# Optimization experiments

Measured on AMD Instinct MI355X. Metric: run time of the kernel, lower is better.

The kernel has to match this reference:

```python
import jax, jax.numpy as jnp
import numpy as np

B, N, D = 4, 4096, 1024

def setup_inputs() -> dict:
    key = jax.random.key(0)
    kx, kql, kqr, kk, kv = jax.random.split(key, 5)
    std = 1.0 / D
    return {
        "x": jax.random.normal(kx, (B, N, D), dtype=jnp.float32),
        "w_query_left": jax.random.normal(kql, (D, D), dtype=jnp.float32) * std,
        "w_query_right": jax.random.normal(kqr, (D, D), dtype=jnp.float32) * std,
        "w_key": jax.random.normal(kk, (D, D), dtype=jnp.float32) * std,
        "w_value": jax.random.normal(kv, (D, D), dtype=jnp.float32) * std,
    }

def reference(x, w_query_left, w_query_right, w_key, w_value):
    # Four dxd projections
    query_left = jnp.einsum('bnd,de->bne', x, w_query_left)
    query_right = jnp.einsum('bnd,de->bne', x, w_query_right)
    key = jnp.einsum('bnd,de->bne', x, w_key)
    value = jnp.einsum('bnd,de->bne', x, w_value)
    # Elementwise gate
    query = query_left * query_right
    # Kernelized attention: key^T @ value, then query @ kv  (dropout p=0 in eval)
    kv_attn = jnp.einsum('bnd,bne->bde', key, value)   # [B, D, D]
    linear_attn = jnp.einsum('bnd,bde->bne', query, kv_attn)
    return linear_attn
```

## Files before the change

### kernel.cpp

```cpp
#include <hip/hip_runtime.h>
#include <stdint.h>

typedef short bf16x8 __attribute__((ext_vector_type(8)));
typedef float f32x4 __attribute__((ext_vector_type(4)));

__device__ __forceinline__ uint16_t f2b(float f) {
    uint32_t u = __builtin_bit_cast(uint32_t, f);
    return (uint16_t)((u + 0x7fffu + ((u >> 16) & 1u)) >> 16);
}

__device__ __forceinline__ void gll16(const void* g, void* l) {
    __builtin_amdgcn_global_load_lds(
        (const __attribute__((address_space(1))) uint32_t*)(uintptr_t)g,
        (__attribute__((address_space(3))) uint32_t*)(uint32_t)(uintptr_t)l,
        16, 0, 0);
}

__device__ __forceinline__ void swz3(int& bx, int& by, int& bz) {
    const int nx = gridDim.x, ny = gridDim.y, nz = gridDim.z;
    const int n = nx * ny * nz;
    int orig = blockIdx.x + nx * (blockIdx.y + ny * blockIdx.z);
    int l = (orig & 7) * (n >> 3) + (orig >> 3);
    bx = l % nx; l /= nx;
    by = l % ny;
    bz = l / ny;
}

struct Ptr4 { const float* p[4]; };

__global__ __launch_bounds__(256) void prep(const float* __restrict__ x,
                                            uint16_t* __restrict__ xb,
                                            uint16_t* __restrict__ xT,
                                            Ptr4 wp, uint16_t* __restrict__ Wt) {
    __shared__ uint16_t tile[64][68];
    const int t = threadIdx.x;
    int id = blockIdx.x;
    if (id < 4096) {
        const int d0 = (id & 15) * 64;
        const int n0 = ((id >> 4) & 63) * 64;
        const int b = id >> 10;
        const float* xbase = x + (size_t)b * 4194304;
#pragma unroll
        for (int p = 0; p < 4; p++) {
            int row = p * 16 + (t >> 4);
            int c4 = (t & 15) * 4;
            float4 v = *(const float4*)&xbase[(size_t)(n0 + row) * 1024 + d0 + c4];
            uint16_t b0 = f2b(v.x), b1 = f2b(v.y), b2 = f2b(v.z), b3 = f2b(v.w);
            tile[row][c4 + 0] = b0;
            tile[row][c4 + 1] = b1;
            tile[row][c4 + 2] = b2;
            tile[row][c4 + 3] = b3;
            uint2 pk;
            pk.x = (uint32_t)b0 | ((uint32_t)b1 << 16);
            pk.y = (uint32_t)b2 | ((uint32_t)b3 << 16);
            *(uint2*)&xb[(size_t)(b * 4096 + n0 + row) * 1024 + d0 + c4] = pk;
        }
        __syncthreads();
        uint16_t* oT = xT + (size_t)b * 4194304;
#pragma unroll
        for (int p = 0; p < 4; p++) {
            int a = p * 16 + (t >> 4);
            int b4 = (t & 15) * 4;
            uint32_t x0 = tile[b4 + 0][a], x1 = tile[b4 + 1][a];
            uint32_t x2 = tile[b4 + 2][a], x3 = tile[b4 + 3][a];
            uint2 pk;
            pk.x = x0 | (x1 << 16);
            pk.y = x2 | (x3 << 16);
            *(uint2*)&oT[(size_t)(d0 + a) * 4096 + n0 + b4] = pk;
        }
    } else {
        id -= 4096;
        const int c0 = (id & 15) * 64;
        const int r0 = ((id >> 4) & 15) * 64;
        const int m = id >> 8;
        const float* in = wp.p[m];
        uint16_t* o = Wt + (size_t)m * 1048576;
#pragma unroll
        for (int p = 0; p < 4; p++) {
            int row = p * 16 + (t >> 4);
            int c4 = (t & 15) * 4;
            float4 v = *(const float4*)&in[(size_t)(r0 + row) * 1024 + c0 + c4];
            tile[row][c4 + 0] = f2b(v.x);
            tile[row][c4 + 1] = f2b(v.y);
            tile[row][c4 + 2] = f2b(v.z);
            tile[row][c4 + 3] = f2b(v.w);
        }
        __syncthreads();
#pragma unroll
        for (int p = 0; p < 4; p++) {
            int a = p * 16 + (t >> 4);
            int b4 = (t & 15) * 4;
            uint32_t x0 = tile[b4 + 0][a], x1 = tile[b4 + 1][a];
            uint32_t x2 = tile[b4 + 2][a], x3 = tile[b4 + 3][a];
            uint2 pk;
            pk.x = x0 | (x1 << 16);
            pk.y = x2 | (x3 << 16);
            *(uint2*)&o[(size_t)(c0 + a) * 1024 + r0 + b4] = pk;
        }
    }
}

__global__ __launch_bounds__(512, 2) void proj_gate8(const uint16_t* __restrict__ A,
                                                     const uint16_t* __restrict__ Wt,
                                                     uint16_t* __restrict__ Q) {
    __shared__ uint16_t lds[65536];
    const int t = threadIdx.x;
    const int wave = t >> 6;
    const int lane = t & 63;
    int bx, by, bz;
    swz3(bx, by, bz);
    const int m0 = by * 256;
    const int e0 = bx * 128;
    const uint16_t* B1 = Wt + (size_t)e0 * 1024;
    const uint16_t* B2 = Wt + 1048576 + (size_t)e0 * 1024;
    const int wm = (wave >> 1) * 64;
    const int wn = (wave & 1) * 64;

    int LsA0 = t * 16;
    int LsA1 = 8192 + t * 16;
    int gbA0 = LsA0 ^ (((LsA0 >> 7) & 7) << 4);
    int gbA1 = LsA1 ^ (((LsA1 >> 7) & 7) << 4);
    int gbB  = gbA0;
    const uint16_t* srcA0 = A + (size_t)(m0 + (gbA0 >> 6)) * 1024 + ((gbA0 & 63) >> 1);
    const uint16_t* srcA1 = A + (size_t)(m0 + (gbA1 >> 6)) * 1024 + ((gbA1 & 63) >> 1);
    const uint16_t* srcB1 = B1 + (size_t)(gbB >> 6) * 1024 + ((gbB & 63) >> 1);
    const uint16_t* srcB2 = B2 + (size_t)(gbB >> 6) * 1024 + ((gbB & 63) >> 1);

    auto STAGE = [&](int kt_, int ks_) {
        const int h = (2 * kt_ + ks_) & 3;
        const int kb = kt_ * 64 + ks_ * 32;
        uint16_t* db = lds + h * 16384 + (wave << 9);
        gll16(srcA0 + kb, db);
        gll16(srcA1 + kb, db + 4096);
        gll16(srcB1 + kb, db + 8192);
        gll16(srcB2 + kb, db + 12288);
    };

    const int cb = (lane >> 4) << 4;
    int aoff[4], b1off[4], b2off[4];
#pragma unroll
    for (int i = 0; i < 4; i++) {
        int g = (wm + i * 16 + (lane & 15)) * 64 + cb;
        aoff[i] = (g ^ (((g >> 7) & 7) << 4)) >> 1;
    }
#pragma unroll
    for (int j = 0; j < 4; j++) {
        int g = (wn + j * 16 + (lane & 15)) * 64 + cb;
        int sw = (g ^ (((g >> 7) & 7) << 4)) >> 1;
        b1off[j] = 8192 + sw;
        b2off[j] = 12288 + sw;
    }

    f32x4 acc1[4][4] = {};
    f32x4 acc2[4][4] = {};

    STAGE(0, 0); STAGE(0, 1); STAGE(1, 0); STAGE(1, 1);
    asm volatile("s_waitcnt vmcnt(12)" ::: "memory");
    __builtin_amdgcn_s_barrier();

    for (int kt = 0; kt < 16; ++kt) {
        const uint16_t* lb0 = lds + ((2 * kt) & 3) * 16384;
        const uint16_t* lb1 = lds + ((2 * kt + 1) & 3) * 16384;
        bf16x8 af[4], bq[4];

#pragma unroll
        for (int i = 0; i < 4; i++) af[i] = *(const bf16x8*)&lb0[aoff[i]];
#pragma unroll
        for (int j = 0; j < 4; j++) bq[j] = *(const bf16x8*)&lb0[b1off[j]];
        __builtin_amdgcn_s_barrier();
        asm volatile("s_waitcnt lgkmcnt(0)" ::: "memory");
        __builtin_amdgcn_sched_barrier(0);
        __builtin_amdgcn_s_setprio(1);
#pragma unroll
        for (int i = 0; i < 4; i++)
#pragma unroll
            for (int j = 0; j < 4; j++)
                acc1[i][j] = __builtin_amdgcn_mfma_f32_16x16x32_bf16(af[i], bq[j],
                                                                     acc1[i][j], 0, 0, 0);
        __builtin_amdgcn_s_setprio(0);
        __builtin_amdgcn_s_barrier();

#pragma unroll
        for (int j = 0; j < 4; j++) bq[j] = *(const bf16x8*)&lb0[b2off[j]];
        __builtin_amdgcn_s_barrier();
        asm volatile("s_waitcnt lgkmcnt(0)" ::: "memory");
        __builtin_amdgcn_sched_barrier(0);
        __builtin_amdgcn_s_setprio(1);
#pragma unroll
        for (int i = 0; i < 4; i++)
#pragma unroll
            for (int j = 0; j < 4; j++)
                acc2[i][j] = __builtin_amdgcn_mfma_f32_16x16x32_bf16(af[i], bq[j],
                                                                     acc2[i][j], 0, 0, 0);
        __builtin_amdgcn_s_setprio(0);
        if (kt < 15) { asm volatile("s_waitcnt vmcnt(8)" ::: "memory"); }
        else         { asm volatile("s_waitcnt vmcnt(0)" ::: "memory"); }
        __builtin_amdgcn_s_barrier();
        if (kt < 14) STAGE(kt + 2, 0);

#pragma unroll
        for (int i = 0; i < 4; i++) af[i] = *(const bf16x8*)&lb1[aoff[i]];
#pragma unroll
        for (int j = 0; j < 4; j++) bq[j] = *(const bf16x8*)&lb1[b1off[j]];
        __builtin_amdgcn_s_barrier();
        asm volatile("s_waitcnt lgkmcnt(0)" ::: "memory");
        __builtin_amdgcn_sched_barrier(0);
        __builtin_amdgcn_s_setprio(1);
#pragma unroll
        for (int i = 0; i < 4; i++)
#pragma unroll
            for (int j = 0; j < 4; j++)
                acc1[i][j] = __builtin_amdgcn_mfma_f32_16x16x32_bf16(af[i], bq[j],
                                                                     acc1[i][j], 0, 0, 0);
        __builtin_amdgcn_s_setprio(0);
        __builtin_amdgcn_s_barrier();

#pragma unroll
        for (int j = 0; j < 4; j++) bq[j] = *(const bf16x8*)&lb1[b2off[j]];
        __builtin_amdgcn_s_barrier();
        asm volatile("s_waitcnt lgkmcnt(0)" ::: "memory");
        __builtin_amdgcn_sched_barrier(0);
        __builtin_amdgcn_s_setprio(1);
#pragma unroll
        for (int i = 0; i < 4; i++)
#pragma unroll
            for (int j = 0; j < 4; j++)
                acc2[i][j] = __builtin_amdgcn_mfma_f32_16x16x32_bf16(af[i], bq[j],
                                                                     acc2[i][j], 0, 0, 0);
        __builtin_amdgcn_s_setprio(0);
        if (kt < 14)       { asm volatile("s_waitcnt vmcnt(8)" ::: "memory"); }
        else if (kt == 14) { asm volatile("s_waitcnt vmcnt(4)" ::: "memory"); }
        else               { asm volatile("s_waitcnt vmcnt(0)" ::: "memory"); }
        __builtin_amdgcn_s_barrier();
        if (kt < 14) STAGE(kt + 2, 1);
    }

    const int rl = (lane >> 4) * 4;
    const int cl = lane & 15;
#pragma unroll
    for (int i = 0; i < 4; i++)
#pragma unroll
        for (int j = 0; j < 4; j++)
#pragma unroll
            for (int r = 0; r < 4; r++) {
                float g = acc1[i][j][r] * acc2[i][j][r];
                Q[(size_t)(m0 + wm + i * 16 + rl + r) * 1024 + e0 + wn + j * 16 + cl] = f2b(g);
            }
}

__global__ __launch_bounds__(512, 2) void gram8(const uint16_t* __restrict__ xT,
                                                float* __restrict__ P) {
    __shared__ uint16_t lds[49152];
    const int t = threadIdx.x;
    const int wave = t >> 6;
    const int lane = t & 63;
    int bx, by, bz;
    swz3(bx, by, bz);
    const int m0 = by * 256;
    const int n0 = bx * 128;
    const int batch = bz >> 1, ks = bz & 1;
    const uint16_t* Xb = xT + (size_t)batch * 4194304 + ks * 2048;
    const int wm = (wave >> 1) * 64;
    const int wn = (wave & 1) * 64;

    int LsA0 = t * 16;
    int LsA1 = 8192 + t * 16;
    int gbA0 = LsA0 ^ (((LsA0 >> 7) & 7) << 4);
    int gbA1 = LsA1 ^ (((LsA1 >> 7) & 7) << 4);
    int gbB  = gbA0;
    const uint16_t* srcA0 = Xb + (size_t)(m0 + (gbA0 >> 6)) * 4096 + ((gbA0 & 63) >> 1);
    const uint16_t* srcA1 = Xb + (size_t)(m0 + (gbA1 >> 6)) * 4096 + ((gbA1 & 63) >> 1);
    const uint16_t* srcB  = Xb + (size_t)(n0 + (gbB  >> 6)) * 4096 + ((gbB  & 63) >> 1);

    auto STAGE = [&](int kt_, int ks2_) {
        const int h = (2 * kt_ + ks2_) & 3;
        const int kb = kt_ * 64 + ks2_ * 32;
        uint16_t* db = lds + h * 12288 + (wave << 9);
        gll16(srcA0 + kb, db);
        gll16(srcA1 + kb, db + 4096);
        gll16(srcB  + kb, db + 8192);
    };

    const int cb = (lane >> 4) << 4;
    int aoff[4], boff[4];
#pragma unroll
    for (int i = 0; i < 4; i++) {
        int g = (wm + i * 16 + (lane & 15)) * 64 + cb;
        aoff[i] = (g ^ (((g >> 7) & 7) << 4)) >> 1;
    }
#pragma unroll
    for (int j = 0; j < 4; j++) {
        int g = (wn + j * 16 + (lane & 15)) * 64 + cb;
        boff[j] = 8192 + ((g ^ (((g >> 7) & 7) << 4)) >> 1);
    }

    f32x4 acc[4][4] = {};

    STAGE(0, 0); STAGE(0, 1); STAGE(1, 0); STAGE(1, 1);
    asm volatile("s_waitcnt vmcnt(9)" ::: "memory");
    __builtin_amdgcn_s_barrier();

    for (int kt = 0; kt < 32; ++kt) {
        const uint16_t* lb0 = lds + ((2 * kt) & 3) * 12288;
        const uint16_t* lb1 = lds + ((2 * kt + 1) & 3) * 12288;
        bf16x8 af[4], bq[4];

#pragma unroll
        for (int i = 0; i < 4; i++) af[i] = *(const bf16x8*)&lb0[aoff[i]];
#pragma unroll
        for (int j = 0; j < 4; j++) bq[j] = *(const bf16x8*)&lb0[boff[j]];
        __builtin_amdgcn_s_barrier();
        asm volatile("s_waitcnt lgkmcnt(0)" ::: "memory");
        __builtin_amdgcn_sched_barrier(0);
        __builtin_amdgcn_s_setprio(1);
#pragma unroll
        for (int i = 0; i < 4; i++)
#pragma unroll
            for (int j = 0; j < 4; j++)
                acc[i][j] = __builtin_amdgcn_mfma_f32_16x16x32_bf16(af[i], bq[j],
                                                                    acc[i][j], 0, 0, 0);
        __builtin_amdgcn_s_setprio(0);
        if (kt < 31) { asm volatile("s_waitcnt vmcnt(6)" ::: "memory"); }
        else         { asm volatile("s_waitcnt vmcnt(0)" ::: "memory"); }
        __builtin_amdgcn_s_barrier();
        if (kt < 30) STAGE(kt + 2, 0);

#pragma unroll
        for (int i = 0; i < 4; i++) af[i] = *(const bf16x8*)&lb1[aoff[i]];
#pragma unroll
        for (int j = 0; j < 4; j++) bq[j] = *(const bf16x8*)&lb1[boff[j]];
        __builtin_amdgcn_s_barrier();
        asm volatile("s_waitcnt lgkmcnt(0)" ::: "memory");
        __builtin_amdgcn_sched_barrier(0);
        __builtin_amdgcn_s_setprio(1);
#pragma unroll
        for (int i = 0; i < 4; i++)
#pragma unroll
            for (int j = 0; j < 4; j++)
                acc[i][j] = __builtin_amdgcn_mfma_f32_16x16x32_bf16(af[i], bq[j],
                                                                    acc[i][j], 0, 0, 0);
        __builtin_amdgcn_s_setprio(0);
        if (kt < 30)       { asm volatile("s_waitcnt vmcnt(6)" ::: "memory"); }
        else if (kt == 30) { asm volatile("s_waitcnt vmcnt(3)" ::: "memory"); }
        else               { asm volatile("s_waitcnt vmcnt(0)" ::: "memory"); }
        __builtin_amdgcn_s_barrier();
        if (kt < 30) STAGE(kt + 2, 1);
    }

    float* Pb = P + (size_t)bz * 1048576;
    const int crow = m0 + wm + (lane >> 4) * 4;
    const int ccol = n0 + wn + (lane & 15);
#pragma unroll
    for (int i = 0; i < 4; i++)
#pragma unroll
        for (int j = 0; j < 4; j++)
#pragma unroll
            for (int r = 0; r < 4; r++)
                Pb[(size_t)(crow + i * 16 + r) * 1024 + ccol + j * 16] = acc[i][j][r];
}

__global__ __launch_bounds__(256) void gemm_h(const uint16_t* __restrict__ WvT,
                                              const float* __restrict__ P,
                                              uint16_t* __restrict__ H) {
    int bxs, bys, bzs;
    swz3(bxs, bys, bzs);
    __shared__ uint16_t lA[4096];
    __shared__ uint16_t lB[4096];

    const int t = threadIdx.x;
    const int wave = t >> 6;
    const int lane = t & 63;
    const int m0 = bys * 128;
    const int n0 = bxs * 128;
    const int wm = (wave >> 1) * 64;
    const int wn = (wave & 1) * 64;

    const uint16_t* gA0 = WvT + (size_t)(m0 + (t >> 2)) * 1024 + (t & 3) * 8;
    uint16_t* lA0 = lA + wave * 512;
    uint16_t* lA1 = lA + 2048 + wave * 512;

    const int row1 = n0 + (t >> 2);
    const int row2 = row1 + 64;
    const float* pb1 = P + (size_t)(row1 >> 10) * 2097152 + (size_t)(row1 & 1023) * 1024 + (t & 3) * 8;
    const float* pb2 = P + (size_t)(row2 >> 10) * 2097152 + (size_t)(row2 & 1023) * 1024 + (t & 3) * 8;
    uint16_t* wB1 = lB + (t >> 2) * 32 + (t & 3) * 8;
    uint16_t* wB2 = lB + 2048 + (t >> 2) * 32 + (t & 3) * 8;

    f32x4 acc[4][4] = {};

    const int arow = wm + (lane & 15);
    const int brow = wn + (lane & 15);
    const int koff = (lane >> 4) * 8;

    for (int k0 = 0; k0 < 1024; k0 += 32) {
        __syncthreads();
        gll16(gA0 + k0, lA0);
        gll16(gA0 + (size_t)64 * 1024 + k0, lA1);
        {
            float4 a0 = *(const float4*)(pb1 + k0);
            float4 a1 = *(const float4*)(pb1 + k0 + 4);
            float4 b0 = *(const float4*)(pb1 + 1048576 + k0);
            float4 b1 = *(const float4*)(pb1 + 1048576 + k0 + 4);
            uint4 v;
            v.x = (uint32_t)f2b(a0.x + b0.x) | ((uint32_t)f2b(a0.y + b0.y) << 16);
            v.y = (uint32_t)f2b(a0.z + b0.z) | ((uint32_t)f2b(a0.w + b0.w) << 16);
            v.z = (uint32_t)f2b(a1.x + b1.x) | ((uint32_t)f2b(a1.y + b1.y) << 16);
            v.w = (uint32_t)f2b(a1.z + b1.z) | ((uint32_t)f2b(a1.w + b1.w) << 16);
            *(uint4*)wB1 = v;
        }
        {
            float4 a0 = *(const float4*)(pb2 + k0);
            float4 a1 = *(const float4*)(pb2 + k0 + 4);
            float4 b0 = *(const float4*)(pb2 + 1048576 + k0);
            float4 b1 = *(const float4*)(pb2 + 1048576 + k0 + 4);
            uint4 v;
            v.x = (uint32_t)f2b(a0.x + b0.x) | ((uint32_t)f2b(a0.y + b0.y) << 16);
            v.y = (uint32_t)f2b(a0.z + b0.z) | ((uint32_t)f2b(a0.w + b0.w) << 16);
            v.z = (uint32_t)f2b(a1.x + b1.x) | ((uint32_t)f2b(a1.y + b1.y) << 16);
            v.w = (uint32_t)f2b(a1.z + b1.z) | ((uint32_t)f2b(a1.w + b1.w) << 16);
            *(uint4*)wB2 = v;
        }
        __syncthreads();

        bf16x8 af[4], bfr[4];
#pragma unroll
        for (int i = 0; i < 4; i++)
            af[i] = *(const bf16x8*)&lA[(arow + i * 16) * 32 + koff];
#pragma unroll
        for (int i = 0; i < 4; i++)
            bfr[i] = *(const bf16x8*)&lB[(brow + i * 16) * 32 + koff];
#pragma unroll
        for (int i = 0; i < 4; i++)
#pragma unroll
            for (int j = 0; j < 4; j++)
                acc[i][j] = __builtin_amdgcn_mfma_f32_16x16x32_bf16(af[i], bfr[j],
                                                                    acc[i][j], 0, 0, 0);
    }

    const int crow = m0 + wm + (lane >> 4) * 4;
    const int ccol = n0 + wn + (lane & 15);
#pragma unroll
    for (int i = 0; i < 4; i++)
#pragma unroll
        for (int j = 0; j < 4; j++)
#pragma unroll
            for (int r = 0; r < 4; r++)
                H[(size_t)(crow + i * 16 + r) * 4096 + ccol + j * 16] = f2b(acc[i][j][r]);
}

__global__ __launch_bounds__(512, 2) void gemm_out8(const uint16_t* __restrict__ A,
                                                    const uint16_t* __restrict__ kvT,
                                                    float* __restrict__ C) {
    __shared__ uint16_t lds[65536];
    const int t = threadIdx.x;
    const int wave = t >> 6;
    const int lane = t & 63;
    int bx, by, bz;
    swz3(bx, by, bz);
    const int m0 = by * 256;
    const int n0 = bx * 256;
    const int batch = by >> 4;
    const uint16_t* Bb = kvT + (size_t)batch * 1048576 + (size_t)n0 * 1024;
    const int wm = (wave >> 2) * 128;
    const int wn = (wave & 3) * 64;

    int Ls0 = t * 16;
    int Ls1 = 8192 + t * 16;
    int gb0 = Ls0 ^ (((Ls0 >> 7) & 7) << 4);
    int gb1 = Ls1 ^ (((Ls1 >> 7) & 7) << 4);
    const uint16_t* srcA0 = A + (size_t)(m0 + (gb0 >> 6)) * 1024 + ((gb0 & 63) >> 1);
    const uint16_t* srcA1 = A + (size_t)(m0 + (gb1 >> 6)) * 1024 + ((gb1 & 63) >> 1);
    const uint16_t* srcB0 = Bb + (size_t)(gb0 >> 6) * 1024 + ((gb0 & 63) >> 1);
    const uint16_t* srcB1 = Bb + (size_t)(gb1 >> 6) * 1024 + ((gb1 & 63) >> 1);

    auto STAGE = [&](int kt_, int ks_) {
        const int h = (2 * kt_ + ks_) & 3;
        const int kb = kt_ * 64 + ks_ * 32;
        uint16_t* db = lds + h * 16384 + (wave << 9);
        gll16(srcA0 + kb, db);
        gll16(srcA1 + kb, db + 4096);
        gll16(srcB0 + kb, db + 8192);
        gll16(srcB1 + kb, db + 12288);
    };

    const int cb = (lane >> 4) << 4;
    int aoff[8], boff[4];
#pragma unroll
    for (int i = 0; i < 8; i++) {
        int g = (wm + i * 16 + (lane & 15)) * 64 + cb;
        aoff[i] = (g ^ (((g >> 7) & 7) << 4)) >> 1;
    }
#pragma unroll
    for (int j = 0; j < 4; j++) {
        int g = (wn + j * 16 + (lane & 15)) * 64 + cb;
        boff[j] = 8192 + ((g ^ (((g >> 7) & 7) << 4)) >> 1);
    }

    f32x4 acc[8][4] = {};

    STAGE(0, 0); STAGE(0, 1); STAGE(1, 0); STAGE(1, 1);
    asm volatile("s_waitcnt vmcnt(12)" ::: "memory");
    __builtin_amdgcn_s_barrier();

    for (int kt = 0; kt < 16; ++kt) {
        const uint16_t* lb0 = lds + ((2 * kt) & 3) * 16384;
        const uint16_t* lb1 = lds + ((2 * kt + 1) & 3) * 16384;
        bf16x8 af[8], bq[4];

#pragma unroll
        for (int i = 0; i < 8; i++) af[i] = *(const bf16x8*)&lb0[aoff[i]];
#pragma unroll
        for (int j = 0; j < 4; j++) bq[j] = *(const bf16x8*)&lb0[boff[j]];
        __builtin_amdgcn_s_barrier();
        asm volatile("s_waitcnt lgkmcnt(0)" ::: "memory");
        __builtin_amdgcn_sched_barrier(0);
        __builtin_amdgcn_s_setprio(1);
#pragma unroll
        for (int i = 0; i < 8; i++)
#pragma unroll
            for (int j = 0; j < 4; j++)
                acc[i][j] = __builtin_amdgcn_mfma_f32_16x16x32_bf16(af[i], bq[j],
                                                                    acc[i][j], 0, 0, 0);
        __builtin_amdgcn_s_setprio(0);
        if (kt < 15) { asm volatile("s_waitcnt vmcnt(8)" ::: "memory"); }
        else         { asm volatile("s_waitcnt vmcnt(0)" ::: "memory"); }
        __builtin_amdgcn_s_barrier();
        if (kt < 14) STAGE(kt + 2, 0);

#pragma unroll
        for (int i = 0; i < 8; i++) af[i] = *(const bf16x8*)&lb1[aoff[i]];
#pragma unroll
        for (int j = 0; j < 4; j++) bq[j] = *(const bf16x8*)&lb1[boff[j]];
        __builtin_amdgcn_s_barrier();
        asm volatile("s_waitcnt lgkmcnt(0)" ::: "memory");
        __builtin_amdgcn_sched_barrier(0);
        __builtin_amdgcn_s_setprio(1);
#pragma unroll
        for (int i = 0; i < 8; i++)
#pragma unroll
            for (int j = 0; j < 4; j++)
                acc[i][j] = __builtin_amdgcn_mfma_f32_16x16x32_bf16(af[i], bq[j],
                                                                    acc[i][j], 0, 0, 0);
        __builtin_amdgcn_s_setprio(0);
        if (kt < 14)       { asm volatile("s_waitcnt vmcnt(8)" ::: "memory"); }
        else if (kt == 14) { asm volatile("s_waitcnt vmcnt(4)" ::: "memory"); }
        else               { asm volatile("s_waitcnt vmcnt(0)" ::: "memory"); }
        __builtin_amdgcn_s_barrier();
        if (kt < 14) STAGE(kt + 2, 1);
    }

    const int rl = (lane >> 4) * 4;
    const int cl = lane & 15;
#pragma unroll
    for (int i = 0; i < 8; i++)
#pragma unroll
        for (int j = 0; j < 4; j++)
#pragma unroll
            for (int r = 0; r < 4; r++)
                C[(size_t)(m0 + wm + i * 16 + rl + r) * 1024 + n0 + wn + j * 16 + cl] =
                    acc[i][j][r];
}

__global__ __launch_bounds__(256) void gemm_nt_bf16(const uint16_t* __restrict__ A,
                                                    int lda, int az,
                                                    const uint16_t* __restrict__ Bt,
                                                    int ldb,
                                                    uint16_t* __restrict__ C,
                                                    int ldc, int cz) {
    int bxs, bys, bzs;
    swz3(bxs, bys, bzs);
    const uint16_t* Ab = A + (size_t)bzs * az;
    uint16_t* Cb = C + (size_t)bzs * cz;

    __shared__ uint16_t lA[4096];
    __shared__ uint16_t lB[4096];

    const int t = threadIdx.x;
    const int wave = t >> 6;
    const int lane = t & 63;
    const int m0 = bys * 128;
    const int n0 = bxs * 128;
    const int wm = (wave >> 1) * 64;
    const int wn = (wave & 1) * 64;

    const uint16_t* gA0 = Ab + (size_t)(m0 + (t >> 2)) * lda + (t & 3) * 8;
    const uint16_t* gB0 = Bt + (size_t)(n0 + (t >> 2)) * ldb + (t & 3) * 8;
    uint16_t* lA0 = lA + wave * 512;
    uint16_t* lA1 = lA + 2048 + wave * 512;
    uint16_t* lB0 = lB + wave * 512;
    uint16_t* lB1 = lB + 2048 + wave * 512;

    f32x4 acc[4][4] = {};

    const int arow = wm + (lane & 15);
    const int brow = wn + (lane & 15);
    const int koff = (lane >> 4) * 8;

    for (int k0 = 0; k0 < 1024; k0 += 32) {
        __syncthreads();
        gll16(gA0 + k0, lA0);
        gll16(gA0 + (size_t)64 * lda + k0, lA1);
        gll16(gB0 + k0, lB0);
        gll16(gB0 + (size_t)64 * ldb + k0, lB1);
        __syncthreads();

        bf16x8 af[4], bfr[4];
#pragma unroll
        for (int i = 0; i < 4; i++)
            af[i] = *(const bf16x8*)&lA[(arow + i * 16) * 32 + koff];
#pragma unroll
        for (int i = 0; i < 4; i++)
            bfr[i] = *(const bf16x8*)&lB[(brow + i * 16) * 32 + koff];
#pragma unroll
        for (int i = 0; i < 4; i++)
#pragma unroll
            for (int j = 0; j < 4; j++)
                acc[i][j] = __builtin_amdgcn_mfma_f32_16x16x32_bf16(af[i], bfr[j],
                                                                    acc[i][j], 0, 0, 0);
    }

    const int crow = m0 + wm + (lane >> 4) * 4;
    const int ccol = n0 + wn + (lane & 15);
#pragma unroll
    for (int i = 0; i < 4; i++)
#pragma unroll
        for (int j = 0; j < 4; j++)
#pragma unroll
            for (int r = 0; r < 4; r++)
                Cb[(size_t)(crow + i * 16 + r) * ldc + ccol + j * 16] = f2b(acc[i][j][r]);
}

extern "C" void kernel_launch(void* const* d_in, const int* in_sizes, int n_in,
                              void* d_out, int out_size, void* d_ws, size_t ws_size,
                              hipStream_t stream) {
    const float* x = (const float*)d_in[0];

    uint16_t* ws  = (uint16_t*)d_ws;
    uint16_t* xb  = ws;
    uint16_t* xT  = ws + 16777216;
    uint16_t* Wt  = ws + 33554432;
    uint16_t* Q   = ws + 37748736;
    float*    P   = (float*)(ws + 54525952);
    uint16_t* H   = ws + 75497472;
    uint16_t* kvT = ws + 79691776;

    Ptr4 wp;
    wp.p[0] = (const float*)d_in[1];
    wp.p[1] = (const float*)d_in[2];
    wp.p[2] = (const float*)d_in[3];
    wp.p[3] = (const float*)d_in[4];
    prep<<<5120, 256, 0, stream>>>(x, xb, xT, wp, Wt);

    proj_gate8<<<dim3(8, 64), 512, 0, stream>>>(xb, Wt, Q);

    gram8<<<dim3(8, 4, 8), 512, 0, stream>>>(xT, P);

    gemm_h<<<dim3(32, 8, 1), 256, 0, stream>>>(Wt + 3 * 1048576, P, H);

    gemm_nt_bf16<<<dim3(8, 8, 4), 256, 0, stream>>>(H, 4096, 1024,
                                                    Wt + 2 * 1048576, 1024,
                                                    kvT, 1024, 1048576);

    gemm_out8<<<dim3(4, 64), 512, 0, stream>>>(Q, kvT, (float*)d_out);
}
```

Baseline: 352.3 us.

## Split partial-Gram reduction into separate kernel and reuse generic NT GEMM

The Gram partial-sum reduction and bf16 conversion move out of the gemm_h inner loop into a standalone reduce_kv kernel that writes a bf16 Gram matrix G. The H GEMM then uses the generic gemm_nt_bf16 path, loading both operands into LDS with global_load_lds. This removes the repeated fp32 loads and conversions of P that each tile of the old kernel did, at the cost of one extra launch and an extra write and read of G. The query projection is also split into two launches of half the row range each, which looks like a tail or scheduling experiment.

```diff
diff --git a/kernel.cpp b/kernel.cpp
--- a/kernel.cpp
+++ b/kernel.cpp
@@ -102,14 +102,15 @@
 
 __global__ __launch_bounds__(512, 2) void proj_gate8(const uint16_t* __restrict__ A,
                                                      const uint16_t* __restrict__ Wt,
-                                                     uint16_t* __restrict__ Q) {
+                                                     uint16_t* __restrict__ Q,
+                                                     int mbase) {
     __shared__ uint16_t lds[65536];
     const int t = threadIdx.x;
     const int wave = t >> 6;
     const int lane = t & 63;
     int bx, by, bz;
     swz3(bx, by, bz);
-    const int m0 = by * 256;
+    const int m0 = mbase + by * 256;
     const int e0 = bx * 128;
     const uint16_t* B1 = Wt + (size_t)e0 * 1024;
     const uint16_t* B2 = Wt + 1048576 + (size_t)e0 * 1024;
@@ -359,11 +360,35 @@
                 Pb[(size_t)(crow + i * 16 + r) * 1024 + ccol + j * 16] = acc[i][j][r];
 }
 
-__global__ __launch_bounds__(256) void gemm_h(const uint16_t* __restrict__ WvT,
-                                              const float* __restrict__ P,
-                                              uint16_t* __restrict__ H) {
+__global__ __launch_bounds__(256) void reduce_kv(const float4* __restrict__ P,
+                                                 uint2* __restrict__ G) {
+    int i = blockIdx.x * 256 + threadIdx.x;
+    int b = i >> 18;
+    int r = i & 262143;
+    const float4* base = P + (size_t)b * 524288 + r;
+    float4 s0 = base[0];
+    float4 s1 = base[262144];
+    float x = s0.x + s1.x;
+    float y = s0.y + s1.y;
+    float zz = s0.z + s1.z;
+    float w = s0.w + s1.w;
+    uint2 o;
+    o.x = (uint32_t)f2b(x) | ((uint32_t)f2b(y) << 16);
+    o.y = (uint32_t)f2b(zz) | ((uint32_t)f2b(w) << 16);
+    G[i] = o;
+}
+
+__global__ __launch_bounds__(256) void gemm_nt_bf16(const uint16_t* __restrict__ A,
+                                                    int lda, int az,
+                                                    const uint16_t* __restrict__ Bt,
+                                                    int ldb,
+                                                    uint16_t* __restrict__ C,
+                                                    int ldc, int cz) {
     int bxs, bys, bzs;
     swz3(bxs, bys, bzs);
+    const uint16_t* Ab = A + (size_t)bzs * az;
+    uint16_t* Cb = C + (size_t)bzs * cz;
+
     __shared__ uint16_t lA[4096];
     __shared__ uint16_t lB[4096];
 
@@ -375,16 +400,12 @@
     const int wm = (wave >> 1) * 64;
     const int wn = (wave & 1) * 64;
 
-    const uint16_t* gA0 = WvT + (size_t)(m0 + (t >> 2)) * 1024 + (t & 3) * 8;
+    const uint16_t* gA0 = Ab + (size_t)(m0 + (t >> 2)) * lda + (t & 3) * 8;
+    const uint16_t* gB0 = Bt + (size_t)(n0 + (t >> 2)) * ldb + (t & 3) * 8;
     uint16_t* lA0 = lA + wave * 512;
     uint16_t* lA1 = lA + 2048 + wave * 512;
-
-    const int row1 = n0 + (t >> 2);
-    const int row2 = row1 + 64;
-    const float* pb1 = P + (size_t)(row1 >> 10) * 2097152 + (size_t)(row1 & 1023) * 1024 + (t & 3) * 8;
-    const float* pb2 = P + (size_t)(row2 >> 10) * 2097152 + (size_t)(row2 & 1023) * 1024 + (t & 3) * 8;
-    uint16_t* wB1 = lB + (t >> 2) * 32 + (t & 3) * 8;
-    uint16_t* wB2 = lB + 2048 + (t >> 2) * 32 + (t & 3) * 8;
+    uint16_t* lB0 = lB + wave * 512;
+    uint16_t* lB1 = lB + 2048 + wave * 512;
 
     f32x4 acc[4][4] = {};
 
@@ -395,31 +416,9 @@
     for (int k0 = 0; k0 < 1024; k0 += 32) {
         __syncthreads();
         gll16(gA0 + k0, lA0);
-        gll16(gA0 + (size_t)64 * 1024 + k0, lA1);
-        {
-            float4 a0 = *(const float4*)(pb1 + k0);
-            float4 a1 = *(const float4*)(pb1 + k0 + 4);
-            float4 b0 = *(const float4*)(pb1 + 1048576 + k0);
-            float4 b1 = *(const float4*)(pb1 + 1048576 + k0 + 4);
-            uint4 v;
-            v.x = (uint32_t)f2b(a0.x + b0.x) | ((uint32_t)f2b(a0.y + b0.y) << 16);
-            v.y = (uint32_t)f2b(a0.z + b0.z) | ((uint32_t)f2b(a0.w + b0.w) << 16);
-            v.z = (uint32_t)f2b(a1.x + b1.x) | ((uint32_t)f2b(a1.y + b1.y) << 16);
-            v.w = (uint32_t)f2b(a1.z + b1.z) | ((uint32_t)f2b(a1.w + b1.w) << 16);
-            *(uint4*)wB1 = v;
-        }
-        {
-            float4 a0 = *(const float4*)(pb2 + k0);
-            float4 a1 = *(const float4*)(pb2 + k0 + 4);
-            float4 b0 = *(const float4*)(pb2 + 1048576 + k0);
-            float4 b1 = *(const float4*)(pb2 + 1048576 + k0 + 4);
-            uint4 v;
-            v.x = (uint32_t)f2b(a0.x + b0.x) | ((uint32_t)f2b(a0.y + b0.y) << 16);
-            v.y = (uint32_t)f2b(a0.z + b0.z) | ((uint32_t)f2b(a0.w + b0.w) << 16);
-            v.z = (uint32_t)f2b(a1.x + b1.x) | ((uint32_t)f2b(a1.y + b1.y) << 16);
-            v.w = (uint32_t)f2b(a1.z + b1.z) | ((uint32_t)f2b(a1.w + b1.w) << 16);
-            *(uint4*)wB2 = v;
-        }
+        gll16(gA0 + (size_t)64 * lda + k0, lA1);
+        gll16(gB0 + k0, lB0);
+        gll16(gB0 + (size_t)64 * ldb + k0, lB1);
         __syncthreads();
 
         bf16x8 af[4], bfr[4];
@@ -445,7 +444,7 @@
         for (int j = 0; j < 4; j++)
 #pragma unroll
             for (int r = 0; r < 4; r++)
-                H[(size_t)(crow + i * 16 + r) * 4096 + ccol + j * 16] = f2b(acc[i][j][r]);
+                Cb[(size_t)(crow + i * 16 + r) * ldc + ccol + j * 16] = f2b(acc[i][j][r]);
 }
 
 __global__ __launch_bounds__(512, 2) void gemm_out8(const uint16_t* __restrict__ A,
@@ -561,75 +560,6 @@
                     acc[i][j][r];
 }
 
-__global__ __launch_bounds__(256) void gemm_nt_bf16(const uint16_t* __restrict__ A,
-                                                    int lda, int az,
-                                                    const uint16_t* __restrict__ Bt,
-                                                    int ldb,
-                                                    uint16_t* __restrict__ C,
-                                                    int ldc, int cz) {
-    int bxs, bys, bzs;
-    swz3(bxs, bys, bzs);
-    const uint16_t* Ab = A + (size_t)bzs * az;
-    uint16_t* Cb = C + (size_t)bzs * cz;
-
-    __shared__ uint16_t lA[4096];
-    __shared__ uint16_t lB[4096];
-
-    const int t = threadIdx.x;
-    const int wave = t >> 6;
-    const int lane = t & 63;
-    const int m0 = bys * 128;
-    const int n0 = bxs * 128;
-    const int wm = (wave >> 1) * 64;
-    const int wn = (wave & 1) * 64;
-
-    const uint16_t* gA0 = Ab + (size_t)(m0 + (t >> 2)) * lda + (t & 3) * 8;
-    const uint16_t* gB0 = Bt + (size_t)(n0 + (t >> 2)) * ldb + (t & 3) * 8;
-    uint16_t* lA0 = lA + wave * 512;
-    uint16_t* lA1 = lA + 2048 + wave * 512;
-    uint16_t* lB0 = lB + wave * 512;
-    uint16_t* lB1 = lB + 2048 + wave * 512;
-
-    f32x4 acc[4][4] = {};
-
-    const int arow = wm + (lane & 15);
-    const int brow = wn + (lane & 15);
-    const int koff = (lane >> 4) * 8;
-
-    for (int k0 = 0; k0 < 1024; k0 += 32) {
-        __syncthreads();
-        gll16(gA0 + k0, lA0);
-        gll16(gA0 + (size_t)64 * lda + k0, lA1);
-        gll16(gB0 + k0, lB0);
-        gll16(gB0 + (size_t)64 * ldb + k0, lB1);
-        __syncthreads();
-
-        bf16x8 af[4], bfr[4];
-#pragma unroll
-        for (int i = 0; i < 4; i++)
-            af[i] = *(const bf16x8*)&lA[(arow + i * 16) * 32 + koff];
-#pragma unroll
-        for (int i = 0; i < 4; i++)
-            bfr[i] = *(const bf16x8*)&lB[(brow + i * 16) * 32 + koff];
-#pragma unroll
-        for (int i = 0; i < 4; i++)
-#pragma unroll
-            for (int j = 0; j < 4; j++)
-                acc[i][j] = __builtin_amdgcn_mfma_f32_16x16x32_bf16(af[i], bfr[j],
-                                                                    acc[i][j], 0, 0, 0);
-    }
-
-    const int crow = m0 + wm + (lane >> 4) * 4;
-    const int ccol = n0 + wn + (lane & 15);
-#pragma unroll
-    for (int i = 0; i < 4; i++)
-#pragma unroll
-        for (int j = 0; j < 4; j++)
-#pragma unroll
-            for (int r = 0; r < 4; r++)
-                Cb[(size_t)(crow + i * 16 + r) * ldc + ccol + j * 16] = f2b(acc[i][j][r]);
-}
-
 extern "C" void kernel_launch(void* const* d_in, const int* in_sizes, int n_in,
                               void* d_out, int out_size, void* d_ws, size_t ws_size,
                               hipStream_t stream) {
@@ -641,6 +571,7 @@
     uint16_t* Wt  = ws + 33554432;
     uint16_t* Q   = ws + 37748736;
     float*    P   = (float*)(ws + 54525952);
+    uint16_t* G   = ws + 71303168;
     uint16_t* H   = ws + 75497472;
     uint16_t* kvT = ws + 79691776;
 
@@ -651,11 +582,15 @@
     wp.p[3] = (const float*)d_in[4];
     prep<<<5120, 256, 0, stream>>>(x, xb, xT, wp, Wt);
 
-    proj_gate8<<<dim3(8, 64), 512, 0, stream>>>(xb, Wt, Q);
+    proj_gate8<<<dim3(8, 32), 512, 0, stream>>>(xb, Wt, Q, 0);
+    proj_gate8<<<dim3(8, 32), 512, 0, stream>>>(xb, Wt, Q, 8192);
 
     gram8<<<dim3(8, 4, 8), 512, 0, stream>>>(xT, P);
 
-    gemm_h<<<dim3(32, 8, 1), 256, 0, stream>>>(Wt + 3 * 1048576, P, H);
+    reduce_kv<<<4096, 256, 0, stream>>>((const float4*)P, (uint2*)G);
+
+    gemm_nt_bf16<<<dim3(32, 8, 1), 256, 0, stream>>>(Wt + 3 * 1048576, 1024, 0,
+                                                     G, 1024, H, 4096, 0);
 
     gemm_nt_bf16<<<dim3(8, 8, 4), 256, 0, stream>>>(H, 4096, 1024,
                                                     Wt + 2 * 1048576, 1024,
```

Measured after the change: 332.8 us. 5.6% less time.
